# Kernel optimization log

Hardware: AMD Instinct MI355X
Metric: run time of the kernel (lower is better)

## Reference

```python
import jax, jax.numpy as jnp
import numpy as np

STEP = 16
LEAK = 32
KSIZE = STEP + LEAK          # 48
PAD = 32                     # ceil((48+16)/2)
THETA = 25.6                 # dense(0.05) * synapses(512) * input_channel(1)
FODEP = 48                   # = kernel_size
BIAS = 0.5
OUT_CH = 1


def setup_inputs() -> dict:
    key = jax.random.key(0)
    k1, k2 = jax.random.split(key, 2)
    input_spikes = (jax.random.uniform(k1, (16, 1, 512, 512)) < 0.05).astype(jnp.float32)
    # weight ~ Exponential(rate=1/w_init) with w_init=0.5, clipped to [0,1]
    u = jax.random.uniform(k2, (1024, 512), minval=1e-6, maxval=1.0)
    weight = jnp.clip(-0.5 * jnp.log(u), 0.0, 1.0)
    return {"input_spikes": input_spikes, "weight": weight}


def _winner_takes_all(potentials):
    # potentials: [B, C, N, T] -> iterate over time with sequential depression state
    p = jnp.transpose(potentials, (3, 1, 0, 2))  # [T, C, B, N]
    T, C, B, N = p.shape

    def step(dep, p_t):
        # dep: [C, B, N] depression counters (integer-valued floats)
        wins = []
        for c in range(C):
            pot = p_t[c] * (dep[c] == 0)                      # mask depressed neurons
            widx = jnp.argmax(pot, axis=-1)                   # [B]
            wval = jnp.take_along_axis(pot, widx[:, None], axis=-1)[:, 0]
            spike = (wval > THETA).astype(pot.dtype)          # [B]
            win = jax.nn.one_hot(widx, N, dtype=pot.dtype) * spike[:, None]  # [B, N]
            # torch: scatter_add(-spike*fodep at winner) then += spike*fodep broadcast
            dep = dep.at[c].add(spike[:, None] * FODEP - win * FODEP)
            # torch: depression += winners[t, c] * fodep (all channels)
            dep = dep + win[None] * FODEP
            wins.append(win)
        dep = jnp.clip(dep - 1.0, 0.0, FODEP - 1.0)
        return dep, jnp.stack(wins, 0)                        # [C, B, N]

    dep0 = jnp.zeros((C, B, N), p.dtype)
    _, winners = jax.lax.scan(step, dep0, p)                  # winners: [T, C, B, N]
    return jnp.transpose(winners, (2, 1, 3, 0))               # [B, C, N, T]


def _forward(input_spikes, weight):
    B, Ci, S, T = input_spikes.shape
    x = input_spikes.reshape(B, Ci * S, T)
    # StepFireLeak.get_weight_kernel
    t = jnp.arange(KSIZE, dtype=weight.dtype)                 # [K]
    t_spike = t / STEP                                        # [K]
    t_leak = -(t - weight[..., None] * STEP) / LEAK + weight[..., None]  # [O, I, K]
    kernel = jnp.maximum(0.0, jnp.minimum(t_spike, t_leak))[..., ::-1]   # [O, I, K] flipped
    pot = jax.lax.conv_general_dilated(
        x, kernel, window_strides=(1,), padding=[(PAD, PAD)],
        dimension_numbers=('NCH', 'OIH', 'NCH'))              # [B, O*N, T']
    N = weight.shape[0] // OUT_CH
    pot = pot.reshape(B, OUT_CH, N, -1) + BIAS * THETA        # labels=None branch
    return _winner_takes_all(pot)


def reference(input_spikes, weight):
    return _forward(input_spikes, weight)
```

## Files before the change

kernel.cpp:

```cpp
#include <hip/hip_runtime.h>
#include <stdint.h>


#define NB 16
#define NI 512
#define NT 512
#define NO 1024
#define TOUT 529
#define SCAP 96
#define OTILE 4
#define PLEN 571
#define ROWF 2284
#define DUST 564u
#define THETA_F 25.6f
#define BIAS_T 12.8f

__global__ __launch_bounds__(256) void k_pre(const float* __restrict__ x,
                                             const float* __restrict__ weight,
                                             unsigned short* __restrict__ slist,
                                             unsigned int* __restrict__ spkw,
                                             unsigned int* __restrict__ counts,
                                             float* __restrict__ hg,
                                             float4* __restrict__ tap) {
    __shared__ __align__(16) char lsd[1024];
    const int bid = blockIdx.x;
    const int tid = threadIdx.x;
    if (bid < 2048) {
        unsigned short (*sls)[SCAP] = (unsigned short(*)[SCAP])lsd;
        int wq = tid >> 6, lane = tid & 63;
        int row = bid * 4 + wq;
        const float* xr = x + (size_t)row * NT;
        for (int j = lane; j < SCAP; j += 64) sls[wq][j] = 0xFFFFu;
        int base = 0;
        for (int kk = 0; kk < 8; ++kk) {
            int t = kk * 64 + lane;
            bool pred = xr[t] > 0.5f;
            unsigned long long mask = __ballot(pred);
            int pre = __popcll(mask & ((1ull << lane) - 1ull));
            int pos = base + pre;
            if (pred && pos < SCAP) sls[wq][pos] = (unsigned short)t;
            base += __popcll(mask);
        }
        __syncthreads();
        if (lane < SCAP / 2) {
            unsigned v = (unsigned)sls[wq][2 * lane] | ((unsigned)sls[wq][2 * lane + 1] << 16);
            ((unsigned int*)(slist + (size_t)row * SCAP))[lane] = v;
        }
        if (lane < 32)
            spkw[(size_t)row * 32 + lane] = (unsigned)sls[wq][lane] | ((unsigned)sls[wq][lane + 32] << 16);
        if (lane == 0) counts[row] = (unsigned)min(base, SCAP);
    } else if (bid < 2176) {
        float* hs = (float*)lsd;
        int bid2 = bid - 2048;
        int b = bid2 >> 3, seg = bid2 & 7;
        int t = seg * 64 + (tid & 63), isub = tid >> 6;
        const float* xb = x + (size_t)b * NI * NT + t;
        float s = 0.f;
        for (int i = isub * 128; i < isub * 128 + 128; ++i) s += xb[(size_t)i * NT];
        hs[tid] = s;
        __syncthreads();
        if (tid < 64)
            hg[b * NT + seg * 64 + tid] = (hs[tid] + hs[tid + 64]) + (hs[tid + 128] + hs[tid + 192]);
    } else {
        int p = (bid - 2176) * 256 + tid;
        int o = p >> 9, i = p & 511;
        float w = weight[o * NI + i];
        float b15 = 1.5f * w;
        float vA1 = 0.f, vA2 = 0.f, vB1 = 0.f, vB2 = 0.f;
        int posA = 2000, posB = 2000, state = 0;
        float Km1 = 0.f, Km2 = 0.f;
        for (int tau = 0; tau <= 49; ++tau) {
            float K = 0.f;
            if (tau <= 47) {
                float f = (float)tau * 0.0625f;
                float g = b15 - (float)tau * 0.03125f;
                K = fmaxf(0.f, fminf(f, g));
            }
            float d = (K - Km1) - (Km1 - Km2);
            if (tau == 1) d -= 0.0625f;
            if (d != 0.f) {
                if (state == 0)      { posA = tau; vA1 = d; state = 1; }
                else if (state == 1) { if (tau == posA + 1) { vA2 = d; state = 2; }
                                       else { posB = tau; vB1 = d; state = 3; } }
                else if (state == 2) { posB = tau; vB1 = d; state = 3; }
                else if (state == 3) { if (tau == posB + 1) { vB2 = d; state = 4; } }
            }
            Km2 = Km1; Km1 = K;
        }
        size_t base = 2 * ((size_t)o * NI + i);
        tap[base]     = make_float4(vA1, vA2, __int_as_float(posA), 0.f);
        tap[base + 1] = make_float4(vB1, vB2, __int_as_float(posB), 0.f);
    }
}

#define PROC(TP, WV, CNT, IDX)                                                        \
    {                                                                                 \
        const int p = __float_as_int((TP).z);                                         \
        {                                                                             \
            unsigned e = min((unsigned)((int)((WV) & 0xFFFFu) + p), DUST);            \
            float* c = accw + e;                                                      \
            float a0 = c[0], a1 = c[PLEN];                                            \
            c[0] = a0 + (TP).x; c[PLEN] = a1 + (TP).y;                                \
        }                                                                             \
        if ((CNT) > 32u) {                                                            \
            unsigned e = min((unsigned)((int)((WV) >> 16) + p), DUST);                \
            float* c = accw + e;                                                      \
            float a0 = c[0], a1 = c[PLEN];                                            \
            c[0] = a0 + (TP).x; c[PLEN] = a1 + (TP).y;                                \
        }                                                                             \
        if ((CNT) > 64u) {                                                            \
            const unsigned short* sr = slist + (size_t)(b * NI + (IDX)) * SCAP;       \
            for (int kk = 64 + k; kk < (int)(CNT); kk += 32) {                        \
                unsigned e = min((unsigned)((int)sr[kk] + p), DUST);                  \
                float* c = accw + e;                                                  \
                float a0 = c[0], a1 = c[PLEN];                                        \
                c[0] = a0 + (TP).x; c[PLEN] = a1 + (TP).y;                            \
            }                                                                         \
        }                                                                             \
    }

__global__ __launch_bounds__(256, 4) void k_scatter(const unsigned short* __restrict__ slist,
                                                    const unsigned int* __restrict__ spkw,
                                                    const unsigned int* __restrict__ counts,
                                                    const float4* __restrict__ tap,
                                                    const float* __restrict__ hg,
                                                    float* __restrict__ pot) {
    __shared__ __align__(16) float acc[OTILE * ROWF];
    __shared__ double pub[512];
    const int o0 = blockIdx.x * OTILE;
    const int b  = blockIdx.y;
    const int tid = threadIdx.x;
    const int w = tid >> 6, lane = tid & 63;
    const int k = lane >> 1, ramp = lane & 1;

    for (int idx = tid; idx < OTILE * ROWF / 4; idx += 256)
        ((float4*)acc)[idx] = make_float4(0.f, 0.f, 0.f, 0.f);
    __syncthreads();

    float* accw = acc + w * ROWF + ramp * (2 * PLEN);
    const unsigned int* wrow = spkw + (size_t)(b * NI) * 32 + k;
    const float4* trow = tap + 2 * (size_t)(o0 + w) * NI + ramp;
    const uint4* crow = (const uint4*)(counts + b * NI);

    float4 ntA = trow[0], ntB = trow[2], ntC = trow[4], ntD = trow[6];
    unsigned nwA = wrow[0], nwB = wrow[32], nwC = wrow[64], nwD = wrow[96];
    uint4 ncc = crow[0];

    const int NIQ = NI / 4;
    for (int iq = 0; iq < NIQ; ++iq) {
        const float4 tA = ntA, tB = ntB, tC = ntC, tD = ntD;
        const unsigned wA = nwA, wB = nwB, wC = nwC, wD = nwD;
        const uint4 cc = ncc;
        if (iq + 1 < NIQ) {
            const float4* tb = trow + (size_t)(iq + 1) * 8;
            ntA = tb[0]; ntB = tb[2]; ntC = tb[4]; ntD = tb[6];
            const unsigned int* wb = wrow + (size_t)(iq + 1) * 128;
            nwA = wb[0]; nwB = wb[32]; nwC = wb[64]; nwD = wb[96];
            ncc = crow[iq + 1];
        }
        const int i0 = iq * 4;
        PROC(tA, wA, cc.x, i0)
        PROC(tB, wB, cc.y, i0 + 1)
        PROC(tC, wC, cc.z, i0 + 2)
        PROC(tD, wD, cc.w, i0 + 3)
    }
    __syncthreads();

    const int q = lane;
    const float* row = acc + w * ROWF;
    const float* hb = hg + b * NT;
    double dsv[9];
    double s1d = 0.0, s2d = 0.0;
#pragma unroll
    for (int r = 0; r < 9; ++r) {
        int e = q * 9 + r;
        double d = 0.0;
        if (e < PLEN) {
            d = (double)row[e] + (double)row[2 * PLEN + e];
            if (e >= 1) {
                d += (double)row[PLEN + e - 1] + (double)row[3 * PLEN + e - 1];
                if (e <= NT) d += 0.0625 * (double)hb[e - 1];
            }
        }
        dsv[r] = d; s1d += d; s2d += s1d;
    }
    pub[2 * tid] = s1d; pub[2 * tid + 1] = s2d;
    __syncthreads();
    if (tid < 4) {
        double c1 = 0.0, c2 = 0.0;
        for (int qq = 0; qq < 64; ++qq) {
            int j = (tid << 6) + qq;
            double S1 = pub[2 * j], S2 = pub[2 * j + 1];
            pub[2 * j] = c1; pub[2 * j + 1] = c2;
            c2 += 9.0 * c1 + S2;
            c1 += S1;
        }
    }
    __syncthreads();
    {
        const double C1 = pub[2 * tid], C2 = pub[2 * tid + 1];
        double a1 = 0.0, a2 = 0.0;
        float* rowW = acc + w * ROWF;
        double av = 0.0;
#pragma unroll
        for (int r = 0; r < 9; ++r) {
            a1 += dsv[r]; a2 += a1;
            int e = q * 9 + r;
            av = C2 + C1 * (double)(r + 1) + a2;
            if (e < PLEN) rowW[e] = (float)av;
        }
    }
    __syncthreads();
    for (int oo = 0; oo < OTILE; ++oo)
        for (int t = tid; t < TOUT; t += 256)
            pot[((size_t)(b * NO + o0 + oo)) * TOUT + t] = acc[oo * ROWF + t + 15] + BIAS_T;
}

__global__ __launch_bounds__(256) void k_argmax(float* __restrict__ pot,
                                                float* __restrict__ aval,
                                                unsigned short* __restrict__ aidx) {
    __shared__ float sv[4][64];
    __shared__ int   si[4][64];
    int b = blockIdx.y;
    int t0 = blockIdx.x * 64;
    int lane = threadIdx.x & 63, grp = threadIdx.x >> 6;
    int t = t0 + lane;
    bool valid = t < TOUT;
    float best = -1.f; int bidx = 0;
    if (valid) {
        for (int od = 0; od < 256; ++od) {
            int o = grp * 256 + od;
            float v = pot[((size_t)(b * NO + o)) * TOUT + t];
            if (v > best) { best = v; bidx = o; }
        }
    }
    sv[grp][lane] = best; si[grp][lane] = bidx;
    __syncthreads();
    if (grp == 0 && valid) {
#pragma unroll
        for (int g = 1; g < 4; ++g) {
            float v = sv[g][lane];
            if (v > best) { best = v; bidx = si[g][lane]; }
        }
        aval[t * NB + b] = best;
        aidx[t * NB + b] = (unsigned short)bidx;
    }
    for (int idx = threadIdx.x; idx < NO * 64; idx += 256) {
        int o = idx >> 6, tt = idx & 63;
        int tz = t0 + tt;
        if (tz < TOUT) pot[((size_t)(b * NO + o)) * TOUT + tz] = 0.f;
    }
}

__global__ __launch_bounds__(256) void k_wta(const float* __restrict__ aval,
                                             const unsigned short* __restrict__ aidx,
                                             float* __restrict__ out) {
    __shared__ float lv[TOUT * NB];
    __shared__ unsigned short li[TOUT * NB];
    for (int idx = threadIdx.x; idx < TOUT * NB; idx += 256) { lv[idx] = aval[idx]; li[idx] = aidx[idx]; }
    __syncthreads();
    int b = threadIdx.x;
    if (b < NB) {
        int r = 0;
        for (int t = 0; t < TOUT; ++t) {
            float v = lv[t * NB + b];
            if (r == 0 && v > THETA_F) {
                int n = (int)li[t * NB + b];
                out[((size_t)(b * NO + n)) * TOUT + t] = 1.0f;
                r = 48;
            }
            r = max(r - 1, 0);
        }
    }
}

extern "C" void kernel_launch(void* const* d_in, const int* in_sizes, int n_in,
                              void* d_out, int out_size, void* d_ws, size_t ws_size,
                              hipStream_t stream) {
    const float* x      = (const float*)d_in[0];
    const float* weight = (const float*)d_in[1];
    float* out = (float*)d_out;
    char* ws = (char*)d_ws;
    unsigned short* slist  = (unsigned short*)(ws);
    unsigned int*   spkw   = (unsigned int*)(ws + 1572864);
    unsigned int*   counts = (unsigned int*)(ws + 2621440);
    float4*         tap    = (float4*)(ws + 2654208);
    float*          hg     = (float*)(ws + 19431424);
    float*          aval   = (float*)(ws + 19464192);
    unsigned short* aidx   = (unsigned short*)(ws + 19498048);

    k_pre<<<4224, 256, 0, stream>>>(x, weight, slist, spkw, counts, hg, tap);
    k_scatter<<<dim3(NO / OTILE, NB), 256, 0, stream>>>(slist, spkw, counts, tap, hg, out);
    k_argmax<<<dim3(9, 16), 256, 0, stream>>>(out, aval, aidx);
    k_wta<<<1, 256, 0, stream>>>(aval, aidx, out);
}
```

Baseline: 548.2 us.

## Fuse argmax into scatter via packed atomicMax keys and interleave accumulator cells

The scatter kernel now reduces its four output rows to a per-(t,b) best value and index, packed into an order-preserving 64-bit key that is merged across blocks with a global atomicMax. The separate argmax kernel, which wrote and then re-read the full potential tensor, is removed, and the output is zeroed with a memset instead. The LDS accumulator moves to interleaved float4 cells so each scatter becomes one float2 read-modify-write, with pre-scaled spike offsets and a bounds check replacing the clamp. Spike words are also transposed so each thread loads them as a single uint4. The costs are 8.5K global atomics per output tile and a different tie-breaking encoding for equal values.

```diff
diff --git a/kernel.cpp b/kernel.cpp
--- a/kernel.cpp
+++ b/kernel.cpp
@@ -9,9 +9,8 @@
 #define TOUT 529
 #define SCAP 96
 #define OTILE 4
-#define PLEN 571
-#define ROWF 2284
-#define DUST 564u
+#define NCELL 562
+#define E4LIM 2248u
 #define THETA_F 25.6f
 #define BIAS_T 12.8f
 
@@ -46,8 +45,11 @@
             unsigned v = (unsigned)sls[wq][2 * lane] | ((unsigned)sls[wq][2 * lane + 1] << 16);
             ((unsigned int*)(slist + (size_t)row * SCAP))[lane] = v;
         }
-        if (lane < 32)
-            spkw[(size_t)row * 32 + lane] = (unsigned)sls[wq][lane] | ((unsigned)sls[wq][lane + 32] << 16);
+        if (lane < 32) {
+            unsigned a = min((unsigned)sls[wq][lane] * 4u, 0xFFFFu);
+            unsigned c = min((unsigned)sls[wq][lane + 32] * 4u, 0xFFFFu);
+            spkw[(((size_t)(row >> 2)) * 32 + lane) * 4 + (row & 3)] = a | (c << 16);
+        }
         if (lane == 0) counts[row] = (unsigned)min(base, SCAP);
     } else if (bid < 2176) {
         float* hs = (float*)lsd;
@@ -88,33 +90,36 @@
             Km2 = Km1; Km1 = K;
         }
         size_t base = 2 * ((size_t)o * NI + i);
-        tap[base]     = make_float4(vA1, vA2, __int_as_float(posA), 0.f);
-        tap[base + 1] = make_float4(vB1, vB2, __int_as_float(posB), 0.f);
+        tap[base]     = make_float4(vA1, vA2, __int_as_float(posA * 4), 0.f);
+        tap[base + 1] = make_float4(vB1, vB2, __int_as_float(posB * 4), 0.f);
     }
 }
 
 #define PROC(TP, WV, CNT, IDX)                                                        \
     {                                                                                 \
-        const int p = __float_as_int((TP).z);                                         \
+        const int p4 = __float_as_int((TP).z);                                        \
         {                                                                             \
-            unsigned e = min((unsigned)((int)((WV) & 0xFFFFu) + p), DUST);            \
-            float* c = accw + e;                                                      \
-            float a0 = c[0], a1 = c[PLEN];                                            \
-            c[0] = a0 + (TP).x; c[PLEN] = a1 + (TP).y;                                \
+            unsigned e4 = ((WV) & 0xFFFFu) + p4;                                      \
+            if (e4 < E4LIM) {                                                         \
+                float2* cell = (float2*)(accw + e4);                                  \
+                float2 v = *cell; v.x += (TP).x; v.y += (TP).y; *cell = v;            \
+            }                                                                         \
         }                                                                             \
         if ((CNT) > 32u) {                                                            \
-            unsigned e = min((unsigned)((int)((WV) >> 16) + p), DUST);                \
-            float* c = accw + e;                                                      \
-            float a0 = c[0], a1 = c[PLEN];                                            \
-            c[0] = a0 + (TP).x; c[PLEN] = a1 + (TP).y;                                \
+            unsigned e4 = ((WV) >> 16) + p4;                                          \
+            if (e4 < E4LIM) {                                                         \
+                float2* cell = (float2*)(accw + e4);                                  \
+                float2 v = *cell; v.x += (TP).x; v.y += (TP).y; *cell = v;            \
+            }                                                                         \
         }                                                                             \
         if ((CNT) > 64u) {                                                            \
             const unsigned short* sr = slist + (size_t)(b * NI + (IDX)) * SCAP;       \
             for (int kk = 64 + k; kk < (int)(CNT); kk += 32) {                        \
-                unsigned e = min((unsigned)((int)sr[kk] + p), DUST);                  \
-                float* c = accw + e;                                                  \
-                float a0 = c[0], a1 = c[PLEN];                                        \
-                c[0] = a0 + (TP).x; c[PLEN] = a1 + (TP).y;                            \
+                unsigned e4 = (unsigned)sr[kk] * 4u + p4;                             \
+                if (e4 < E4LIM) {                                                     \
+                    float2* cell = (float2*)(accw + e4);                              \
+                    float2 v = *cell; v.x += (TP).x; v.y += (TP).y; *cell = v;        \
+                }                                                                     \
             }                                                                         \
         }                                                                             \
     }
@@ -124,8 +129,8 @@
                                                     const unsigned int* __restrict__ counts,
                                                     const float4* __restrict__ tap,
                                                     const float* __restrict__ hg,
-                                                    float* __restrict__ pot) {
-    __shared__ __align__(16) float acc[OTILE * ROWF];
+                                                    unsigned long long* __restrict__ akey) {
+    __shared__ float4 acc[OTILE * NCELL];
     __shared__ double pub[512];
     const int o0 = blockIdx.x * OTILE;
     const int b  = blockIdx.y;
@@ -133,41 +138,39 @@
     const int w = tid >> 6, lane = tid & 63;
     const int k = lane >> 1, ramp = lane & 1;
 
-    for (int idx = tid; idx < OTILE * ROWF / 4; idx += 256)
-        ((float4*)acc)[idx] = make_float4(0.f, 0.f, 0.f, 0.f);
-    __syncthreads();
-
-    float* accw = acc + w * ROWF + ramp * (2 * PLEN);
-    const unsigned int* wrow = spkw + (size_t)(b * NI) * 32 + k;
+    for (int idx = tid; idx < OTILE * NCELL; idx += 256) acc[idx] = make_float4(0.f, 0.f, 0.f, 0.f);
+    __syncthreads();
+
+    float* accw = (float*)(acc + w * NCELL) + ramp * 2;
+    const uint4* wrow = (const uint4*)spkw + (size_t)(b * 128) * 32 + k;
     const float4* trow = tap + 2 * (size_t)(o0 + w) * NI + ramp;
     const uint4* crow = (const uint4*)(counts + b * NI);
 
     float4 ntA = trow[0], ntB = trow[2], ntC = trow[4], ntD = trow[6];
-    unsigned nwA = wrow[0], nwB = wrow[32], nwC = wrow[64], nwD = wrow[96];
+    uint4 nwv = wrow[0];
     uint4 ncc = crow[0];
 
     const int NIQ = NI / 4;
     for (int iq = 0; iq < NIQ; ++iq) {
         const float4 tA = ntA, tB = ntB, tC = ntC, tD = ntD;
-        const unsigned wA = nwA, wB = nwB, wC = nwC, wD = nwD;
+        const uint4 wv = nwv;
         const uint4 cc = ncc;
         if (iq + 1 < NIQ) {
             const float4* tb = trow + (size_t)(iq + 1) * 8;
             ntA = tb[0]; ntB = tb[2]; ntC = tb[4]; ntD = tb[6];
-            const unsigned int* wb = wrow + (size_t)(iq + 1) * 128;
-            nwA = wb[0]; nwB = wb[32]; nwC = wb[64]; nwD = wb[96];
+            nwv = wrow[(size_t)(iq + 1) * 32];
             ncc = crow[iq + 1];
         }
         const int i0 = iq * 4;
-        PROC(tA, wA, cc.x, i0)
-        PROC(tB, wB, cc.y, i0 + 1)
-        PROC(tC, wC, cc.z, i0 + 2)
-        PROC(tD, wD, cc.w, i0 + 3)
+        PROC(tA, wv.x, cc.x, i0)
+        PROC(tB, wv.y, cc.y, i0 + 1)
+        PROC(tC, wv.z, cc.z, i0 + 2)
+        PROC(tD, wv.w, cc.w, i0 + 3)
     }
     __syncthreads();
 
     const int q = lane;
-    const float* row = acc + w * ROWF;
+    const float4* rowQ = acc + w * NCELL;
     const float* hb = hg + b * NT;
     double dsv[9];
     double s1d = 0.0, s2d = 0.0;
@@ -175,10 +178,12 @@
     for (int r = 0; r < 9; ++r) {
         int e = q * 9 + r;
         double d = 0.0;
-        if (e < PLEN) {
-            d = (double)row[e] + (double)row[2 * PLEN + e];
+        if (e < 561) {
+            float4 c = rowQ[e];
+            d = (double)c.x + (double)c.z;
             if (e >= 1) {
-                d += (double)row[PLEN + e - 1] + (double)row[3 * PLEN + e - 1];
+                float4 cm = rowQ[e - 1];
+                d += (double)cm.y + (double)cm.w;
                 if (e <= NT) d += 0.0625 * (double)hb[e - 1];
             }
         }
@@ -200,64 +205,41 @@
     {
         const double C1 = pub[2 * tid], C2 = pub[2 * tid + 1];
         double a1 = 0.0, a2 = 0.0;
-        float* rowW = acc + w * ROWF;
-        double av = 0.0;
+        float4* rowW = acc + w * NCELL;
 #pragma unroll
         for (int r = 0; r < 9; ++r) {
             a1 += dsv[r]; a2 += a1;
             int e = q * 9 + r;
-            av = C2 + C1 * (double)(r + 1) + a2;
-            if (e < PLEN) rowW[e] = (float)av;
-        }
-    }
-    __syncthreads();
-    for (int oo = 0; oo < OTILE; ++oo)
-        for (int t = tid; t < TOUT; t += 256)
-            pot[((size_t)(b * NO + o0 + oo)) * TOUT + t] = acc[oo * ROWF + t + 15] + BIAS_T;
-}
-
-__global__ __launch_bounds__(256) void k_argmax(float* __restrict__ pot,
-                                                float* __restrict__ aval,
-                                                unsigned short* __restrict__ aidx) {
-    __shared__ float sv[4][64];
-    __shared__ int   si[4][64];
-    int b = blockIdx.y;
-    int t0 = blockIdx.x * 64;
-    int lane = threadIdx.x & 63, grp = threadIdx.x >> 6;
-    int t = t0 + lane;
-    bool valid = t < TOUT;
-    float best = -1.f; int bidx = 0;
-    if (valid) {
-        for (int od = 0; od < 256; ++od) {
-            int o = grp * 256 + od;
-            float v = pot[((size_t)(b * NO + o)) * TOUT + t];
-            if (v > best) { best = v; bidx = o; }
-        }
-    }
-    sv[grp][lane] = best; si[grp][lane] = bidx;
-    __syncthreads();
-    if (grp == 0 && valid) {
+            if (e < 561) rowW[e].x = (float)(C2 + C1 * (double)(r + 1) + a2);
+        }
+    }
+    __syncthreads();
+    for (int t = tid; t < TOUT; t += 256) {
+        float best = acc[t + 15].x; int bi = 0;
 #pragma unroll
-        for (int g = 1; g < 4; ++g) {
-            float v = sv[g][lane];
-            if (v > best) { best = v; bidx = si[g][lane]; }
-        }
-        aval[t * NB + b] = best;
-        aidx[t * NB + b] = (unsigned short)bidx;
-    }
-    for (int idx = threadIdx.x; idx < NO * 64; idx += 256) {
-        int o = idx >> 6, tt = idx & 63;
-        int tz = t0 + tt;
-        if (tz < TOUT) pot[((size_t)(b * NO + o)) * TOUT + tz] = 0.f;
-    }
-}
-
-__global__ __launch_bounds__(256) void k_wta(const float* __restrict__ aval,
-                                             const unsigned short* __restrict__ aidx,
+        for (int oo = 1; oo < OTILE; ++oo) {
+            float v = acc[oo * NCELL + t + 15].x;
+            if (v > best) { best = v; bi = oo; }
+        }
+        float val = best + BIAS_T;
+        unsigned fb = __float_as_uint(val);
+        unsigned k32 = (fb & 0x80000000u) ? ~fb : (fb | 0x80000000u);
+        unsigned long long key = ((unsigned long long)k32 << 10) | (unsigned)(1023 - (o0 + bi));
+        atomicMax(&akey[t * NB + b], key);
+    }
+}
+
+__global__ __launch_bounds__(256) void k_wta(const unsigned long long* __restrict__ akey,
                                              float* __restrict__ out) {
     __shared__ float lv[TOUT * NB];
     __shared__ unsigned short li[TOUT * NB];
-    for (int idx = threadIdx.x; idx < TOUT * NB; idx += 256) { lv[idx] = aval[idx]; li[idx] = aidx[idx]; }
+    for (int idx = threadIdx.x; idx < TOUT * NB; idx += 256) {
+        unsigned long long key = akey[idx];
+        unsigned k32 = (unsigned)(key >> 10);
+        unsigned fb = (k32 & 0x80000000u) ? (k32 & 0x7FFFFFFFu) : ~k32;
+        lv[idx] = __uint_as_float(fb);
+        li[idx] = (unsigned short)(1023u - (unsigned)(key & 1023u));
+    }
     __syncthreads();
     int b = threadIdx.x;
     if (b < NB) {
@@ -286,11 +268,11 @@
     unsigned int*   counts = (unsigned int*)(ws + 2621440);
     float4*         tap    = (float4*)(ws + 2654208);
     float*          hg     = (float*)(ws + 19431424);
-    float*          aval   = (float*)(ws + 19464192);
-    unsigned short* aidx   = (unsigned short*)(ws + 19498048);
+    unsigned long long* akey = (unsigned long long*)(ws + 19464192);
 
     k_pre<<<4224, 256, 0, stream>>>(x, weight, slist, spkw, counts, hg, tap);
-    k_scatter<<<dim3(NO / OTILE, NB), 256, 0, stream>>>(slist, spkw, counts, tap, hg, out);
-    k_argmax<<<dim3(9, 16), 256, 0, stream>>>(out, aval, aidx);
-    k_wta<<<1, 256, 0, stream>>>(aval, aidx, out);
-}
+    hipMemsetAsync(akey, 0, TOUT * NB * sizeof(unsigned long long), stream);
+    hipMemsetAsync(d_out, 0, (size_t)out_size * sizeof(float), stream);
+    k_scatter<<<dim3(NO / OTILE, NB), 256, 0, stream>>>(slist, spkw, counts, tap, hg, akey);
+    k_wta<<<1, 256, 0, stream>>>(akey, out);
+}
```

Result: faster. 521.2 us (-4.9%).
